# Optimization experiments

Hardware: AMD Instinct MI355X
Metric: run time of the kernel (lower is better)

The kernel has to match this reference:

```python
import jax, jax.numpy as jnp
import numpy as np

B, N, C, H = 8, 2048, 512, 8
D = C // H  # head_dim = 64

def rope(t):
    # t: (B, H, T, D); rotate even/odd interleaved pairs
    T = t.shape[2]
    inv_freq = 1.0 / (10000.0 ** (jnp.arange(0, D, 2, dtype=t.dtype) / D))  # (D/2,)
    pos = jnp.arange(T, dtype=t.dtype)
    freqs = pos[:, None] * inv_freq[None, :]            # (T, D/2)
    cos, sin = jnp.cos(freqs), jnp.sin(freqs)           # broadcast over (B,H)
    t_un = t[..., 0::2]
    t_ev = t[..., 1::2]
    r_un = t_un * cos - t_ev * sin
    r_ev = t_un * sin + t_ev * cos
    # interleave back: (..., D/2, 2) -> (..., D)
    return jnp.stack([r_un, r_ev], axis=-1).reshape(t.shape)

def setup_inputs() -> dict:
    key = jax.random.key(0)
    k1, k2, k3, k4 = jax.random.split(key, 4)
    x = jax.random.normal(k1, (B, N, C), dtype=jnp.float32)
    mask = jax.random.normal(k2, (B, N), dtype=jnp.float32)
    W_qkv = jax.random.normal(k3, (3 * C, C), dtype=jnp.float32) * (1.0 / np.sqrt(C))
    W_proj = jax.random.normal(k4, (C, C), dtype=jnp.float32) * (1.0 / np.sqrt(C))
    b_proj = jnp.zeros((C,), dtype=jnp.float32)
    return {"x": x, "mask": mask, "W_qkv": W_qkv, "W_proj": W_proj,
            "b_proj": b_proj, "num_cls_token": 1}

def reference(x, mask, W_qkv, W_proj, b_proj, num_cls_token):
    scale = D ** (-0.5)
    qkv = jnp.einsum('bnc,fc->bnf', x, W_qkv)             # (B,N,3C)
    qkv = qkv.reshape(B, N, 3, H, D).transpose(2, 0, 3, 1, 4)  # (3,B,H,N,D)
    q, k, v = qkv[0], qkv[1], qkv[2]
    nc = num_cls_token
    if nc > 0:
        q = jnp.concatenate([q[:, :, :nc], rope(q[:, :, nc:])], axis=2)
        k = jnp.concatenate([k[:, :, :nc], rope(k[:, :, nc:])], axis=2)
    else:
        q, k = rope(q), rope(k)
    attn = jnp.einsum('bhnd,bhmd->bhnm', q * scale, k)    # (B,H,N,N)
    attn = attn + mask[:, None, None, :] + mask[:, None, :, None]
    attn = jax.nn.softmax(attn, axis=-1)
    out = jnp.einsum('bhnm,bhmd->bhnd', attn, v)          # (B,H,N,D)
    out = out.transpose(0, 2, 1, 3).reshape(B, N, C)
    return out @ W_proj.T + b_proj
```

## Files before the change

kernel.cpp:

```cpp
#include <hip/hip_runtime.h>
#include <cmath>

#define BB 8
#define NN 2048
#define CC 512
#define HH 8
#define DD 64
#define FF 1536
#define MM (BB*NN)

typedef _Float16 half_t;
typedef __attribute__((ext_vector_type(8))) _Float16 half8;
typedef __attribute__((ext_vector_type(4))) _Float16 half4;
typedef __attribute__((ext_vector_type(2))) __fp16 fp16x2;
typedef __attribute__((ext_vector_type(4))) float floatx4;
typedef __attribute__((ext_vector_type(16))) float floatx16;
typedef __attribute__((ext_vector_type(4))) float fx4;

#define LOG2E 1.44269504088896f
#define EXP2_OFF 4.3280851f

typedef const __attribute__((address_space(1))) unsigned int* gas_ptr;
typedef __attribute__((address_space(3))) unsigned int* las_ptr;
__device__ __forceinline__ void gld16(const half_t* g, half_t* l) {
  __builtin_amdgcn_global_load_lds((gas_ptr)g, (las_ptr)l, 16, 0, 0);
}

#define N1 (MM * CC / 8)
#define N2 (FF * CC / 8)
#define N3 (CC * CC / 8)
#define NC (N1 + N2 + N3)
#define NR (NN * 32)
#define NPREP (NC + NR + MM)
__global__ __launch_bounds__(256) void prep_kernel(
    const float* __restrict__ x, const float* __restrict__ wq,
    const float* __restrict__ wp, const float* __restrict__ mask,
    half_t* __restrict__ d, float2* __restrict__ tab, float* __restrict__ msb) {
  int i = blockIdx.x * 256 + threadIdx.x;
  if (i < NC) {
    const float* s;
    if (i < N1)            s = x  + (size_t)i * 8;
    else if (i < N1 + N2)  s = wq + (size_t)(i - N1) * 8;
    else                   s = wp + (size_t)(i - N1 - N2) * 8;
    float4 a = ((const float4*)s)[0], b = ((const float4*)s)[1];
    half8 h;
    h[0] = (half_t)a.x; h[1] = (half_t)a.y; h[2] = (half_t)a.z; h[3] = (half_t)a.w;
    h[4] = (half_t)b.x; h[5] = (half_t)b.y; h[6] = (half_t)b.z; h[7] = (half_t)b.w;
    ((half8*)d)[i] = h;
  } else if (i < NC + NR) {
    int e = i - NC;
    int p = e >> 5, j = e & 31;
    float ang = (float)p * __powf(10000.0f, -(float)(2 * j) * (1.0f / 64.0f));
    float sv, cv;
    __sincosf(ang, &sv, &cv);
    tab[e] = make_float2(cv, sv);
  } else {
    int k = i - NC - NR;
    msb[k] = mask[k] * LOG2E - EXP2_OFF;
  }
}

__global__ __launch_bounds__(256) void qkv_mfma_kernel(
    const half_t* __restrict__ Ah,
    const half_t* __restrict__ Bh,
    const int*   __restrict__ ncp,
    const float2* __restrict__ tab,
    half_t* __restrict__ Qh, half_t* __restrict__ Kh, half_t* __restrict__ Vt)
{
  __shared__ union {
    struct { half_t A[128 * 32]; half_t B[128 * 32]; } s;
    half_t T[4][64 * 68];
  } sm;

  const int tid  = threadIdx.x;
  const int wave = tid >> 6, lane = tid & 63;
  const int L15  = lane & 15, quad = lane >> 4;
  const int wm = (wave & 1) * 64, wn = (wave >> 1) * 64;
  const int m0 = blockIdx.x * 128;
  const int f0 = blockIdx.y * 128;

  const int srow = lane >> 2;
  const int scolh = (lane & 3) * 8;
  const half_t* Ag = Ah + (size_t)(m0 + wave * 16 + srow) * CC + scolh;
  const half_t* Bg = Bh + (size_t)(f0 + wave * 16 + srow) * CC + scolh;
  half_t* Al = &sm.s.A[(wave * 16) * 32];
  half_t* Bl = &sm.s.B[(wave * 16) * 32];

  floatx4 acc[4][4];
#pragma unroll
  for (int i = 0; i < 4; ++i)
#pragma unroll
    for (int j = 0; j < 4; ++j) acc[i][j] = (floatx4){0.f, 0.f, 0.f, 0.f};

  for (int k0 = 0; k0 < CC; k0 += 32) {
    __syncthreads();
    gld16(Ag + k0,            Al);
    gld16(Ag + k0 + 64 * CC,  Al + 64 * 32);
    gld16(Bg + k0,            Bl);
    gld16(Bg + k0 + 64 * CC,  Bl + 64 * 32);
    __syncthreads();
    half8 af[4], bf[4];
#pragma unroll
    for (int mi = 0; mi < 4; ++mi)
      af[mi] = *(const half8*)&sm.s.A[(wm + mi * 16 + L15) * 32 + quad * 8];
#pragma unroll
    for (int ni = 0; ni < 4; ++ni)
      bf[ni] = *(const half8*)&sm.s.B[(wn + ni * 16 + L15) * 32 + quad * 8];
#pragma unroll
    for (int mi = 0; mi < 4; ++mi)
#pragma unroll
      for (int ni = 0; ni < 4; ++ni)
        acc[mi][ni] = __builtin_amdgcn_mfma_f32_16x16x32_f16(bf[ni], af[mi], acc[mi][ni], 0, 0, 0);
  }

  const int which = f0 >> 9;
  const int b     = m0 >> 11;
  const int n_base = (m0 & 2047) + wm;
  const int h     = ((f0 + wn) >> 6) & 7;

  if (which < 2) {
    const int nc = *ncp;
    half_t* dst = which ? Kh : Qh;
    const float qscale = which ? 1.0f : (0.125f * LOG2E);
    const float* tabf = (const float*)tab;
#pragma unroll
    for (int mi = 0; mi < 4; ++mi) {
      const int n = n_base + mi * 16 + L15;
      const int p = n - nc;
      const size_t rbase = (((size_t)(b * HH + h) * NN + n) << 6) + quad * 4;
#pragma unroll
      for (int ni = 0; ni < 4; ++ni) {
        float o0 = acc[mi][ni][0], o1 = acc[mi][ni][1];
        float o2 = acc[mi][ni][2], o3 = acc[mi][ni][3];
        if (p >= 0) {
          const fx4 c4 = *(const fx4*)(tabf + p * 64 + ni * 16 + quad * 4);
          const float e0 = o0, e1 = o1, e2 = o2, e3 = o3;
          o0 = e0 * c4[0] - e1 * c4[1];
          o1 = e0 * c4[1] + e1 * c4[0];
          o2 = e2 * c4[2] - e3 * c4[3];
          o3 = e2 * c4[3] + e3 * c4[2];
        }
        half4 hv;
        hv[0] = (half_t)(o0 * qscale); hv[1] = (half_t)(o1 * qscale);
        hv[2] = (half_t)(o2 * qscale); hv[3] = (half_t)(o3 * qscale);
        *(half4*)(dst + rbase + ni * 16) = hv;
      }
    }
  } else {
    __syncthreads();
#pragma unroll
    for (int ni = 0; ni < 4; ++ni)
#pragma unroll
      for (int mi = 0; mi < 4; ++mi)
#pragma unroll
        for (int r = 0; r < 4; ++r)
          sm.T[wave][(ni * 16 + quad * 4 + r) * 68 + mi * 16 + L15] = (half_t)acc[mi][ni][r];
    __syncthreads();
    const size_t gbase = ((size_t)(b * HH + h) * DD + lane) * NN + n_base;
#pragma unroll
    for (int c = 0; c < 8; ++c)
      *(half8*)(Vt + gbase + c * 8) = *(const half8*)&sm.T[wave][lane * 68 + c * 8];
  }
}

__global__ __launch_bounds__(256, 4) void flash_mfma_kernel(
    const half_t* __restrict__ Qh,
    const half_t* __restrict__ Kh,
    const half_t* __restrict__ Vt,
    const float*  __restrict__ ms,
    half_t* __restrict__ O)
{
  __shared__ half_t KV[2][2][64 * 64];

  const int tid  = threadIdx.x;
  const int wave = tid >> 6;
  const int lane = tid & 63;
  const int l31  = lane & 31;
  const int hi   = lane >> 5;
  const int l7   = lane & 7;

  const int bid  = blockIdx.x;
  const int xcd  = bid & 7;
  const int slot = bid >> 3;
  const int qt   = slot & 15;
  const int head = (slot >> 4) * 8 + xcd;
  const int b    = head >> 3;
  const int h    = head & 7;

  const half_t* Kt_base = Kh + ((((size_t)b * HH + h) * NN) << 6);
  const half_t* Vt_base = Vt + (((size_t)b * HH + h) * DD) * NN;

  half8 qf[4];
  {
    const half_t* Qp =
        Qh + ((((size_t)b * HH + h) * NN + qt * 128 + wave * 32 + l31) << 6) + hi * 8;
#pragma unroll
    for (int kd = 0; kd < 4; ++kd) qf[kd] = *(const half8*)(Qp + kd * 16);
  }

  const int r8  = lane >> 3;
  const int dof = ((l7 ^ r8) << 3);
  const half_t* kbase = Kt_base + (((size_t)(wave * 16 + r8)) << 6) + dof;
  const half_t* vbase = Vt_base + (size_t)(wave * 16 + r8) * NN + dof;

  int adK[4], adV[4];
#pragma unroll
  for (int c = 0; c < 4; ++c) {
    adK[c] = l31 * 128 + ((((c << 1) | hi) ^ l7) << 4);
    adV[c] = 8192 + l31 * 128 + ((((c << 1) | hi) ^ l7) << 4);
  }
  const char* L = (const char*)KV;

  floatx16 acc[2];
#pragma unroll
  for (int dt = 0; dt < 2; ++dt)
#pragma unroll
    for (int r = 0; r < 16; ++r) acc[dt][r] = 0.f;
  float l4[4] = {0.f, 0.f, 0.f, 0.f};

  const float* mkb = ms + (size_t)b * NN + hi * 4;

#define STAGE(c, koff, voff)                                                  \
  {                                                                           \
    gld16(kbase + (koff),          &KV[c][0][wave * 1024]);                   \
    gld16(kbase + (koff) + 512,    &KV[c][0][wave * 1024 + 512]);             \
    gld16(vbase + (voff),          &KV[c][1][wave * 1024]);                   \
    gld16(vbase + (voff) + 8 * NN, &KV[c][1][wave * 1024 + 512]);             \
  }

#define COMPUTE(c, moff)                                                      \
  _Pragma("unroll")                                                           \
  for (int t = 0; t < 2; ++t) {                                               \
    floatx16 S;                                                               \
    _Pragma("unroll")                                                         \
    for (int r2 = 0; r2 < 4; ++r2) {                                          \
      fx4 mv = *(const fx4*)(mkb + (moff) + t * 32 + r2 * 8);                 \
      S[r2 * 4 + 0] = mv[0]; S[r2 * 4 + 1] = mv[1];                           \
      S[r2 * 4 + 2] = mv[2]; S[r2 * 4 + 3] = mv[3];                           \
    }                                                                         \
    __builtin_amdgcn_s_setprio(1);                                            \
    _Pragma("unroll")                                                         \
    for (int kd = 0; kd < 4; ++kd) {                                          \
      half8 kf = *(const half8*)(L + (adK[kd] + (c) * 16384 + t * 4096));     \
      S = __builtin_amdgcn_mfma_f32_32x32x16_f16(kf, qf[kd], S, 0, 0, 0);     \
    }                                                                         \
    __builtin_amdgcn_s_setprio(0);                                            \
    _Pragma("unroll")                                                         \
    for (int r = 0; r < 16; ++r) {                                            \
      float p = __builtin_amdgcn_exp2f(S[r]);                                 \
      l4[r & 3] += p;                                                         \
      S[r] = p;                                                               \
    }                                                                         \
    unsigned W[4][2];                                                         \
    _Pragma("unroll")                                                         \
    for (int r2 = 0; r2 < 4; ++r2)                                            \
      _Pragma("unroll")                                                       \
      for (int u = 0; u < 2; ++u) {                                           \
        union { fp16x2 h; unsigned w; } pk;                                   \
        pk.h = __builtin_amdgcn_cvt_pkrtz(S[r2 * 4 + 2 * u],                  \
                                          S[r2 * 4 + 2 * u + 1]);             \
        W[r2][u] = pk.w;                                                      \
      }                                                                       \
    _Pragma("unroll")                                                         \
    for (int ksl = 0; ksl < 2; ++ksl) {                                       \
      unsigned A0 = W[2 * ksl][0],     A1 = W[2 * ksl][1];                    \
      unsigned B0 = W[2 * ksl + 1][0], B1 = W[2 * ksl + 1][1];                \
        \
        \
      asm("v_permlane32_swap_b32 %0, %1" : "+v"(A0), "+v"(B0));               \
      asm("v_permlane32_swap_b32 %0, %1" : "+v"(A1), "+v"(B1));               \
      union { unsigned u4[4]; half8 v; } pw;                                  \
      pw.u4[0] = A0; pw.u4[1] = A1; pw.u4[2] = B0; pw.u4[3] = B1;             \
      const int ks = t * 2 + ksl;                                             \
      __builtin_amdgcn_s_setprio(1);                                          \
      _Pragma("unroll")                                                       \
      for (int dt = 0; dt < 2; ++dt) {                                        \
        half8 vf = *(const half8*)(L + (adV[ks] + (c) * 16384 + dt * 4096));  \
        acc[dt] = __builtin_amdgcn_mfma_f32_32x32x16_f16(pw.v, vf, acc[dt], 0, 0, 0); \
      }                                                                       \
      __builtin_amdgcn_s_setprio(0);                                          \
    }                                                                         \
  }

  STAGE(0, 0, 0)
  STAGE(1, 4096, 64)
  asm volatile("s_waitcnt vmcnt(4)");
  __builtin_amdgcn_s_barrier();
  __builtin_amdgcn_sched_barrier(0);
  kbase += 8192; vbase += 128;

#pragma unroll 1
  for (int kt2 = 0; kt2 < 15; ++kt2) {
    COMPUTE(0, 0)
    __builtin_amdgcn_sched_barrier(0);
    __builtin_amdgcn_s_barrier();
    STAGE(0, 0, 0)
    asm volatile("s_waitcnt vmcnt(4)");
    __builtin_amdgcn_s_barrier();
    __builtin_amdgcn_sched_barrier(0);

    COMPUTE(1, 64)
    __builtin_amdgcn_sched_barrier(0);
    __builtin_amdgcn_s_barrier();
    STAGE(1, 4096, 64)
    asm volatile("s_waitcnt vmcnt(4)");
    __builtin_amdgcn_s_barrier();
    __builtin_amdgcn_sched_barrier(0);

    kbase += 8192; vbase += 128;
    mkb += 128;
  }

  COMPUTE(0, 0)
  asm volatile("s_waitcnt vmcnt(0)");
  __builtin_amdgcn_s_barrier();
  __builtin_amdgcn_sched_barrier(0);
  COMPUTE(1, 64)

#undef STAGE
#undef COMPUTE

  float l_part = (l4[0] + l4[1]) + (l4[2] + l4[3]);
  l_part += __shfl_xor(l_part, 32, 64);

  const size_t orow = (size_t)b * NN + qt * 128 + wave * 32;
#pragma unroll
  for (int r = 0; r < 16; ++r) {
    const int ql  = (r & 3) + 8 * (r >> 2) + 4 * hi;
    const float iv = 1.0f / __shfl(l_part, ql, 64);
    const size_t ro = ((orow + ql) << 9) + (h << 6) + l31;
    O[ro]      = (half_t)(acc[0][r] * iv);
    O[ro + 32] = (half_t)(acc[1][r] * iv);
  }
}

__global__ __launch_bounds__(256) void proj_mfma_kernel(
    const half_t* __restrict__ Ah,
    const half_t* __restrict__ Bh,
    const float* __restrict__ bias,
    float* __restrict__ out)
{
  __shared__ half_t As[128 * 32];
  __shared__ half_t Bs[64 * 32];

  const int tid  = threadIdx.x;
  const int wave = tid >> 6, lane = tid & 63;
  const int L15  = lane & 15, quad = lane >> 4;
  const int wm = (wave & 1) * 64, wn = (wave >> 1) * 32;
  const int m0 = blockIdx.x * 128;
  const int f0 = blockIdx.y * 64;

  const int srow = lane >> 2;
  const int scolh = (lane & 3) * 8;
  const half_t* Ag = Ah + (size_t)(m0 + wave * 16 + srow) * CC + scolh;
  const half_t* Bg = Bh + (size_t)(f0 + wave * 16 + srow) * CC + scolh;
  half_t* Al = &As[(wave * 16) * 32];
  half_t* Bl = &Bs[(wave * 16) * 32];

  floatx4 acc[4][2];
#pragma unroll
  for (int i = 0; i < 4; ++i)
#pragma unroll
    for (int j = 0; j < 2; ++j) acc[i][j] = (floatx4){0.f, 0.f, 0.f, 0.f};

  for (int k0 = 0; k0 < CC; k0 += 32) {
    __syncthreads();
    gld16(Ag + k0,           Al);
    gld16(Ag + k0 + 64 * CC, Al + 64 * 32);
    gld16(Bg + k0,           Bl);
    __syncthreads();
    half8 af[4], bf[2];
#pragma unroll
    for (int mi = 0; mi < 4; ++mi)
      af[mi] = *(const half8*)&As[(wm + mi * 16 + L15) * 32 + quad * 8];
#pragma unroll
    for (int ni = 0; ni < 2; ++ni)
      bf[ni] = *(const half8*)&Bs[(wn + ni * 16 + L15) * 32 + quad * 8];
#pragma unroll
    for (int mi = 0; mi < 4; ++mi)
#pragma unroll
      for (int ni = 0; ni < 2; ++ni)
        acc[mi][ni] = __builtin_amdgcn_mfma_f32_16x16x32_f16(af[mi], bf[ni], acc[mi][ni], 0, 0, 0);
  }

#pragma unroll
  for (int ni = 0; ni < 2; ++ni) {
    const int f = f0 + wn + ni * 16 + L15;
    const float bv = bias[f];
#pragma unroll
    for (int mi = 0; mi < 4; ++mi)
#pragma unroll
      for (int r = 0; r < 4; ++r)
        out[(size_t)(m0 + wm + mi * 16 + quad * 4 + r) * CC + f] = acc[mi][ni][r] + bv;
  }
}

extern "C" void kernel_launch(void* const* d_in, const int* in_sizes, int n_in,
                              void* d_out, int out_size, void* d_ws, size_t ws_size,
                              hipStream_t stream) {
  const float* x     = (const float*)d_in[0];
  const float* mask  = (const float*)d_in[1];
  const float* Wqkv  = (const float*)d_in[2];
  const float* Wproj = (const float*)d_in[3];
  const float* bproj = (const float*)d_in[4];
  const int*   ncp   = (const int*)d_in[5];
  float* out = (float*)d_out;

  const size_t per = (size_t)BB * HH * NN * DD;
  half_t* xh  = (half_t*)d_ws;
  half_t* Wqh = xh + (size_t)MM * CC;
  half_t* Wph = Wqh + (size_t)FF * CC;
  half_t* Qh  = Wph + (size_t)CC * CC;
  half_t* Kh  = Qh + per;
  half_t* Vt  = Kh + per;
  half_t* Oh  = Vt + per;
  float2* tab = (float2*)(Oh + per);
  float*  msb = (float*)(tab + (size_t)NN * 32);

  prep_kernel<<<dim3(NPREP / 256), 256, 0, stream>>>(x, Wqkv, Wproj, mask, xh, tab, msb);

  qkv_mfma_kernel<<<dim3(MM / 128, FF / 128), 256, 0, stream>>>(xh, Wqh, ncp, tab, Qh, Kh, Vt);
  flash_mfma_kernel<<<dim3(BB * HH * (NN / 128)), 256, 0, stream>>>(Qh, Kh, Vt, msb, Oh);
  proj_mfma_kernel<<<dim3(MM / 128, CC / 64), 256, 0, stream>>>(Oh, Wph, bproj, out);
}
```

Measured before the change: 252.8 us.

## Double-buffer LDS tiles in QKV and projection GEMMs to overlap loads

Converts the QKV and output-projection GEMM mainloops from single-buffered load/sync/compute to a two-stage LDS ping-pong. Global-to-LDS loads for the next K slice are issued while MFMAs run on the current buffer, with vmcnt waits and raw s_barrier in place of __syncthreads, plus setprio around the MFMAs. The aim is to hide global memory latency in the GEMMs. It doubles LDS for the tiles, which could reduce occupancy, and the hand-placed waitcnts add correctness risk.

```diff
diff --git a/kernel.cpp b/kernel.cpp
--- a/kernel.cpp
+++ b/kernel.cpp
@@ -68,7 +68,7 @@
     half_t* __restrict__ Qh, half_t* __restrict__ Kh, half_t* __restrict__ Vt)
 {
   __shared__ union {
-    struct { half_t A[128 * 32]; half_t B[128 * 32]; } s;
+    struct { half_t A[2][128 * 32]; half_t B[2][128 * 32]; } s;
     half_t T[4][64 * 68];
   } sm;
 
@@ -83,8 +83,6 @@
   const int scolh = (lane & 3) * 8;
   const half_t* Ag = Ah + (size_t)(m0 + wave * 16 + srow) * CC + scolh;
   const half_t* Bg = Bh + (size_t)(f0 + wave * 16 + srow) * CC + scolh;
-  half_t* Al = &sm.s.A[(wave * 16) * 32];
-  half_t* Bl = &sm.s.B[(wave * 16) * 32];
 
   floatx4 acc[4][4];
 #pragma unroll
@@ -92,26 +90,66 @@
 #pragma unroll
     for (int j = 0; j < 4; ++j) acc[i][j] = (floatx4){0.f, 0.f, 0.f, 0.f};
 
-  for (int k0 = 0; k0 < CC; k0 += 32) {
-    __syncthreads();
-    gld16(Ag + k0,            Al);
-    gld16(Ag + k0 + 64 * CC,  Al + 64 * 32);
-    gld16(Bg + k0,            Bl);
-    gld16(Bg + k0 + 64 * CC,  Bl + 64 * 32);
-    __syncthreads();
-    half8 af[4], bf[4];
-#pragma unroll
-    for (int mi = 0; mi < 4; ++mi)
-      af[mi] = *(const half8*)&sm.s.A[(wm + mi * 16 + L15) * 32 + quad * 8];
-#pragma unroll
-    for (int ni = 0; ni < 4; ++ni)
-      bf[ni] = *(const half8*)&sm.s.B[(wn + ni * 16 + L15) * 32 + quad * 8];
-#pragma unroll
-    for (int mi = 0; mi < 4; ++mi)
-#pragma unroll
-      for (int ni = 0; ni < 4; ++ni)
-        acc[mi][ni] = __builtin_amdgcn_mfma_f32_16x16x32_f16(bf[ni], af[mi], acc[mi][ni], 0, 0, 0);
-  }
+#define QSTAGE(c, koff)                                                       \
+  {                                                                           \
+    gld16(Ag + (koff),           &sm.s.A[c][(wave * 16) * 32]);               \
+    gld16(Ag + (koff) + 64 * CC, &sm.s.A[c][(64 + wave * 16) * 32]);          \
+    gld16(Bg + (koff),           &sm.s.B[c][(wave * 16) * 32]);               \
+    gld16(Bg + (koff) + 64 * CC, &sm.s.B[c][(64 + wave * 16) * 32]);          \
+  }
+
+#define QCOMPUTE(c)                                                           \
+  {                                                                           \
+    half8 af[4], bf[4];                                                       \
+    _Pragma("unroll")                                                         \
+    for (int mi = 0; mi < 4; ++mi)                                            \
+      af[mi] = *(const half8*)&sm.s.A[c][(wm + mi * 16 + L15) * 32 + quad * 8]; \
+    _Pragma("unroll")                                                         \
+    for (int ni = 0; ni < 4; ++ni)                                            \
+      bf[ni] = *(const half8*)&sm.s.B[c][(wn + ni * 16 + L15) * 32 + quad * 8]; \
+    __builtin_amdgcn_s_setprio(1);                                            \
+    _Pragma("unroll")                                                         \
+    for (int mi = 0; mi < 4; ++mi)                                            \
+      _Pragma("unroll")                                                       \
+      for (int ni = 0; ni < 4; ++ni)                                          \
+        acc[mi][ni] = __builtin_amdgcn_mfma_f32_16x16x32_f16(bf[ni], af[mi], acc[mi][ni], 0, 0, 0); \
+    __builtin_amdgcn_s_setprio(0);                                            \
+  }
+
+  QSTAGE(0, 0)
+  QSTAGE(1, 32)
+  asm volatile("s_waitcnt vmcnt(4)");
+  __builtin_amdgcn_s_barrier();
+  __builtin_amdgcn_sched_barrier(0);
+
+  int k0 = 64;
+#pragma unroll 1
+  for (int kk = 0; kk < 7; ++kk) {
+    QCOMPUTE(0)
+    __builtin_amdgcn_sched_barrier(0);
+    __builtin_amdgcn_s_barrier();
+    QSTAGE(0, k0)
+    asm volatile("s_waitcnt vmcnt(4)");
+    __builtin_amdgcn_s_barrier();
+    __builtin_amdgcn_sched_barrier(0);
+
+    QCOMPUTE(1)
+    __builtin_amdgcn_sched_barrier(0);
+    __builtin_amdgcn_s_barrier();
+    QSTAGE(1, k0 + 32)
+    asm volatile("s_waitcnt vmcnt(4)");
+    __builtin_amdgcn_s_barrier();
+    __builtin_amdgcn_sched_barrier(0);
+    k0 += 64;
+  }
+  QCOMPUTE(0)
+  asm volatile("s_waitcnt vmcnt(0)");
+  __builtin_amdgcn_s_barrier();
+  __builtin_amdgcn_sched_barrier(0);
+  QCOMPUTE(1)
+
+#undef QSTAGE
+#undef QCOMPUTE
 
   const int which = f0 >> 9;
   const int b     = m0 >> 11;
@@ -265,8 +303,6 @@
     for (int ksl = 0; ksl < 2; ++ksl) {                                       \
       unsigned A0 = W[2 * ksl][0],     A1 = W[2 * ksl][1];                    \
       unsigned B0 = W[2 * ksl + 1][0], B1 = W[2 * ksl + 1][1];                \
-        \
-        \
       asm("v_permlane32_swap_b32 %0, %1" : "+v"(A0), "+v"(B0));               \
       asm("v_permlane32_swap_b32 %0, %1" : "+v"(A1), "+v"(B1));               \
       union { unsigned u4[4]; half8 v; } pw;                                  \
@@ -340,8 +376,8 @@
     const float* __restrict__ bias,
     float* __restrict__ out)
 {
-  __shared__ half_t As[128 * 32];
-  __shared__ half_t Bs[64 * 32];
+  __shared__ half_t As[2][128 * 32];
+  __shared__ half_t Bs[2][64 * 32];
 
   const int tid  = threadIdx.x;
   const int wave = tid >> 6, lane = tid & 63;
@@ -354,8 +390,6 @@
   const int scolh = (lane & 3) * 8;
   const half_t* Ag = Ah + (size_t)(m0 + wave * 16 + srow) * CC + scolh;
   const half_t* Bg = Bh + (size_t)(f0 + wave * 16 + srow) * CC + scolh;
-  half_t* Al = &As[(wave * 16) * 32];
-  half_t* Bl = &Bs[(wave * 16) * 32];
 
   floatx4 acc[4][2];
 #pragma unroll
@@ -363,25 +397,65 @@
 #pragma unroll
     for (int j = 0; j < 2; ++j) acc[i][j] = (floatx4){0.f, 0.f, 0.f, 0.f};
 
-  for (int k0 = 0; k0 < CC; k0 += 32) {
-    __syncthreads();
-    gld16(Ag + k0,           Al);
-    gld16(Ag + k0 + 64 * CC, Al + 64 * 32);
-    gld16(Bg + k0,           Bl);
-    __syncthreads();
-    half8 af[4], bf[2];
-#pragma unroll
-    for (int mi = 0; mi < 4; ++mi)
-      af[mi] = *(const half8*)&As[(wm + mi * 16 + L15) * 32 + quad * 8];
-#pragma unroll
-    for (int ni = 0; ni < 2; ++ni)
-      bf[ni] = *(const half8*)&Bs[(wn + ni * 16 + L15) * 32 + quad * 8];
-#pragma unroll
-    for (int mi = 0; mi < 4; ++mi)
-#pragma unroll
-      for (int ni = 0; ni < 2; ++ni)
-        acc[mi][ni] = __builtin_amdgcn_mfma_f32_16x16x32_f16(af[mi], bf[ni], acc[mi][ni], 0, 0, 0);
-  }
+#define PSTAGE(c, koff)                                                       \
+  {                                                                           \
+    gld16(Ag + (koff),           &As[c][(wave * 16) * 32]);                   \
+    gld16(Ag + (koff) + 64 * CC, &As[c][(64 + wave * 16) * 32]);              \
+    gld16(Bg + (koff),           &Bs[c][(wave * 16) * 32]);                   \
+  }
+
+#define PCOMPUTE(c)                                                           \
+  {                                                                           \
+    half8 af[4], bf[2];                                                       \
+    _Pragma("unroll")                                                         \
+    for (int mi = 0; mi < 4; ++mi)                                            \
+      af[mi] = *(const half8*)&As[c][(wm + mi * 16 + L15) * 32 + quad * 8];   \
+    _Pragma("unroll")                                                         \
+    for (int ni = 0; ni < 2; ++ni)                                            \
+      bf[ni] = *(const half8*)&Bs[c][(wn + ni * 16 + L15) * 32 + quad * 8];   \
+    __builtin_amdgcn_s_setprio(1);                                            \
+    _Pragma("unroll")                                                         \
+    for (int mi = 0; mi < 4; ++mi)                                            \
+      _Pragma("unroll")                                                       \
+      for (int ni = 0; ni < 2; ++ni)                                          \
+        acc[mi][ni] = __builtin_amdgcn_mfma_f32_16x16x32_f16(af[mi], bf[ni], acc[mi][ni], 0, 0, 0); \
+    __builtin_amdgcn_s_setprio(0);                                            \
+  }
+
+  PSTAGE(0, 0)
+  PSTAGE(1, 32)
+  asm volatile("s_waitcnt vmcnt(3)");
+  __builtin_amdgcn_s_barrier();
+  __builtin_amdgcn_sched_barrier(0);
+
+  int k0 = 64;
+#pragma unroll 1
+  for (int kk = 0; kk < 7; ++kk) {
+    PCOMPUTE(0)
+    __builtin_amdgcn_sched_barrier(0);
+    __builtin_amdgcn_s_barrier();
+    PSTAGE(0, k0)
+    asm volatile("s_waitcnt vmcnt(3)");
+    __builtin_amdgcn_s_barrier();
+    __builtin_amdgcn_sched_barrier(0);
+
+    PCOMPUTE(1)
+    __builtin_amdgcn_sched_barrier(0);
+    __builtin_amdgcn_s_barrier();
+    PSTAGE(1, k0 + 32)
+    asm volatile("s_waitcnt vmcnt(3)");
+    __builtin_amdgcn_s_barrier();
+    __builtin_amdgcn_sched_barrier(0);
+    k0 += 64;
+  }
+  PCOMPUTE(0)
+  asm volatile("s_waitcnt vmcnt(0)");
+  __builtin_amdgcn_s_barrier();
+  __builtin_amdgcn_sched_barrier(0);
+  PCOMPUTE(1)
+
+#undef PSTAGE
+#undef PCOMPUTE
 
 #pragma unroll
   for (int ni = 0; ni < 2; ++ni) {
```

Measured after the change: 249.2 us. About the same (-1.4%).
